# Kernel tuning notes

Hardware: AMD Instinct MI355X
Metric: run time of the kernel (lower is better)

Reference implementation:

```python
import jax, jax.numpy as jnp
import numpy as np

INV_L_MIN, INV_L_MAX = 0.5, 2.0

def _gelu(x):
    return jax.nn.gelu(x, approximate=False)

def _scaled_sigmoid(x, lo, hi):
    return lo + (hi - lo) * jax.nn.sigmoid(x)

def _fourier_bases(nodes, modes):
    # nodes: [b, n, d]; modes: [k, d, w] -> temp: [b, n, k, w]
    temp = 2.0 * jnp.pi * jnp.einsum('bxd,kdw->bxkw', nodes, modes)
    return jnp.cos(temp), jnp.sin(temp), jnp.ones_like(temp[:, :, :1, :])

def _spectral_conv(x, wc, ws, w0, bc, bs, b0, wbc, wbs, wb0):
    # x: [b, c_in, n]; forward non-uniform Fourier transform via weighted bases
    x_c = jnp.einsum('bix,bxkw->bikw', x, wbc)
    x_s = -jnp.einsum('bix,bxkw->bikw', x, wbs)
    x_0 = jnp.einsum('bix,bxkw->bikw', x, wb0)
    f_c = jnp.einsum('bikw,iokw->bokw', x_c, wc) - jnp.einsum('bikw,iokw->bokw', x_s, ws)
    f_s = jnp.einsum('bikw,iokw->bokw', x_s, wc) + jnp.einsum('bikw,iokw->bokw', x_c, ws)
    f_0 = jnp.einsum('bikw,iokw->bokw', x_0, w0)
    return (jnp.einsum('bokw,bxkw->box', f_0, b0)
            + 2.0 * jnp.einsum('bokw,bxkw->box', f_c, bc)
            - 2.0 * jnp.einsum('bokw,bxkw->box', f_s, bs))


def setup_inputs() -> dict:
    key = jax.random.key(0)
    ks = jax.random.split(key, 32)
    B, NU, NV = 4, 65536, 16384
    K, D, W = 32, 2, 1          # nmodes, ndims, nmeasures
    C, L = 64, 3                # channels, number of BNO layers
    FC, IU, IV, OUT = 128, 2, 3, 1
    f32 = jnp.float32
    rn = lambda k, s, sc=1.0: (sc * jax.random.normal(k, s, dtype=f32))
    ru = lambda k, s, sc=1.0: (sc * jax.random.uniform(k, s, dtype=f32))
    sp_scale = 1.0 / (C * C)
    inp = {
        'u': rn(ks[0], (B, NU, IU)),
        'v': rn(ks[1], (B, NV, IV)),
        'node_mask_u': jnp.ones((B, NU, 1), dtype=jnp.int32),
        'nodes_u': ru(ks[2], (B, NU, D)),
        'nodes_v': ru(ks[3], (B, NV, D)),
        'node_weights_u': ru(ks[4], (B, NU, W), 1.0 / NU),
        'node_weights_v': ru(ks[5], (B, NV, W), 1.0 / NV),
        'modes': ru(ks[6], (K, D, W), 8.0),
        # scaled_logit(1.0, 0.5, 2.0) = log((1-0.5)/(2-1)) = log(0.5)
        'inv_L_scale_latent': jnp.full((D, W), -0.69314718, dtype=f32),
        'fc0_u_w': rn(ks[7], (C, IU), 0.5), 'fc0_u_b': rn(ks[8], (C,), 0.1),
        'fc0_v_w': rn(ks[9], (C, IV), 0.5), 'fc0_v_b': rn(ks[10], (C,), 0.1),
        'sp_ext_wc': ru(ks[11], (L, C, C, K, W), sp_scale),
        'sp_ext_ws': ru(ks[12], (L, C, C, K, W), sp_scale),
        'sp_ext_w0': ru(ks[13], (L, C, C, 1, W), sp_scale),
        'sp_u_wc': ru(ks[14], (L, C, C, K, W), sp_scale),
        'sp_u_ws': ru(ks[15], (L, C, C, K, W), sp_scale),
        'sp_u_w0': ru(ks[16], (L, C, C, 1, W), sp_scale),
        'sp_v_wc': ru(ks[17], (L, C, C, K, W), sp_scale),
        'sp_v_ws': ru(ks[18], (L, C, C, K, W), sp_scale),
        'sp_v_w0': ru(ks[19], (L, C, C, 1, W), sp_scale),
        'ws_u_w': rn(ks[20], (L, C, C), 0.05), 'ws_u_b': rn(ks[21], (L, C), 0.02),
        'ws_v_w': rn(ks[22], (L, C, C), 0.05), 'ws_v_b': rn(ks[23], (L, C), 0.02),
        'fc1_w': rn(ks[24], (FC, C), 0.05), 'fc1_b': rn(ks[25], (FC,), 0.02),
        'fc2_w': rn(ks[26], (OUT, FC), 0.05), 'fc2_b': rn(ks[27], (OUT,), 0.02),
    }
    return inp


def reference(u, v, node_mask_u, nodes_u, nodes_v, node_weights_u, node_weights_v,
              modes, inv_L_scale_latent, fc0_u_w, fc0_u_b, fc0_v_w, fc0_v_b,
              sp_ext_wc, sp_ext_ws, sp_ext_w0, sp_u_wc, sp_u_ws, sp_u_w0,
              sp_v_wc, sp_v_ws, sp_v_w0, ws_u_w, ws_u_b, ws_v_w, ws_v_b,
              fc1_w, fc1_b, fc2_w, fc2_b):
    # node_mask_u is unpacked but unused in the original forward
    m = modes * _scaled_sigmoid(inv_L_scale_latent, INV_L_MIN, INV_L_MAX)  # [k,d,w]
    bc_u, bs_u, b0_u = _fourier_bases(nodes_u, m)
    bc_v, bs_v, b0_v = _fourier_bases(nodes_v, m)
    wu = node_weights_u[:, :, None, :]  # [b,x,1,w]
    wv = node_weights_v[:, :, None, :]
    wbc_u, wbs_u, wb0_u = bc_u * wu, bs_u * wu, b0_u * wu
    wbc_v, wbs_v, wb0_v = bc_v * wv, bs_v * wv, b0_v * wv
    # lift to channel dim and move to [b, c, n]
    u = jnp.einsum('bxi,oi->box', u, fc0_u_w) + fc0_u_b[None, :, None]
    v = jnp.einsum('bxi,oi->box', v, fc0_v_w) + fc0_v_b[None, :, None]
    L = ws_u_w.shape[0]
    for i in range(L):
        u1 = _spectral_conv(v, sp_ext_wc[i], sp_ext_ws[i], sp_ext_w0[i],
                            bc_u, bs_u, b0_u, wbc_v, wbs_v, wb0_v)
        u2 = _spectral_conv(u, sp_u_wc[i], sp_u_ws[i], sp_u_w0[i],
                            bc_u, bs_u, b0_u, wbc_u, wbs_u, wb0_u)
        u3 = jnp.einsum('oi,bix->box', ws_u_w[i], u) + ws_u_b[i][None, :, None]
        u = u1 + u2 + u3
        if i != L - 1:  # v is only updated on non-final layers, as in the original
            u = _gelu(u)
            v1 = _spectral_conv(v, sp_v_wc[i], sp_v_ws[i], sp_v_w0[i],
                                bc_v, bs_v, b0_v, wbc_v, wbs_v, wb0_v)
            v2 = jnp.einsum('oi,bix->box', ws_v_w[i], v) + ws_v_b[i][None, :, None]
            v = _gelu(v1 + v2)
    u = jnp.transpose(u, (0, 2, 1))  # [b, n, c]
    u = _gelu(u @ fc1_w.T + fc1_b)
    return u @ fc2_w.T + fc2_b
```

## Files before the change

### kernel.cpp

```cpp
#include <hip/hip_runtime.h>
#include <math.h>

#define PI2 6.283185307179586f

typedef __attribute__((ext_vector_type(8))) short bf16x8;
typedef __attribute__((ext_vector_type(4))) float f32x4;

__device__ __forceinline__ float gelu_f(float x) {
    return 0.5f * x * (1.0f + erff(x * 0.7071067811865476f));
}
__device__ __forceinline__ unsigned short f2bf(float f) {
    unsigned int u = __float_as_uint(f);
    u += 0x7FFFu + ((u >> 16) & 1u);
    return (unsigned short)(u >> 16);
}
__device__ __forceinline__ float bf2f(unsigned short h) {
    return __uint_as_float(((unsigned int)h) << 16);
}
__device__ __forceinline__ unsigned int pk(unsigned short a, unsigned short b) {
    return (unsigned int)a | ((unsigned int)b << 16);
}
__device__ __forceinline__ void wsplit(float w, unsigned short* dst) {
    unsigned short h = f2bf(w);
    dst[0] = h;
    dst[128] = f2bf(w - bf2f(h));
}

template<int NIN>
__global__ __launch_bounds__(256) void k_prep(const float* __restrict__ nodes, const float* __restrict__ modes,
                                              const float* __restrict__ latent, const float* __restrict__ nw,
                                              const float* __restrict__ inp, const float* __restrict__ fcw,
                                              const float* __restrict__ fcb,
                                              unsigned short* __restrict__ FT, unsigned short* __restrict__ wbb,
                                              unsigned short* __restrict__ chbf, int N) {
    int b = blockIdx.y;
    int x = blockIdx.x * 256 + threadIdx.x;
    float s0 = 0.5f + 1.5f / (1.0f + expf(-latent[0]));
    float s1 = 0.5f + 1.5f / (1.0f + expf(-latent[1]));
    float n0 = nodes[((size_t)b * N + x) * 2 + 0];
    float n1 = nodes[((size_t)b * N + x) * 2 + 1];
    float wx = nw[(size_t)b * N + x];
    unsigned short* wb = wbb + (size_t)b * 65 * N + x;
    unsigned int row[64];
    #pragma unroll
    for (int k = 0; k < 32; ++k) {
        float m0 = modes[k * 2 + 0] * s0;
        float m1 = modes[k * 2 + 1] * s1;
        float t = PI2 * (n0 * m0 + n1 * m1);
        float s, c;
        sincosf(t, &s, &c);
        unsigned short hc = f2bf(c), hs = f2bf(s);
        if (k & 1) { row[k >> 1] |= ((unsigned int)hc << 16); row[16 + (k >> 1)] |= ((unsigned int)hs << 16); }
        else       { row[k >> 1] = hc;                         row[16 + (k >> 1)] = hs; }
        wb[(size_t)k * N] = f2bf(c * wx);
        wb[(size_t)(32 + k) * N] = f2bf(s * wx);
    }
    wb[(size_t)64 * N] = f2bf(wx);
    float xi[NIN];
    #pragma unroll
    for (int i = 0; i < NIN; ++i) xi[i] = inp[((size_t)b * N + x) * NIN + i];
    unsigned short* cb = chbf + (size_t)b * 64 * N + x;
    #pragma unroll
    for (int c = 0; c < 64; ++c) {
        float a = fcb[c];
        #pragma unroll
        for (int i = 0; i < NIN; ++i) a += fcw[c * NIN + i] * xi[i];
        unsigned short h = f2bf(a);
        cb[(size_t)c * N] = h;
        if (c & 1) row[32 + (c >> 1)] |= ((unsigned int)h << 16);
        else row[32 + (c >> 1)] = h;
    }
    unsigned int* fr = (unsigned int*)(FT + ((size_t)b * N + x) * 128);
    #pragma unroll
    for (int i = 0; i < 64; ++i) fr[i] = row[i];
}

__global__ __launch_bounds__(256) void k_analysis2(const unsigned short* __restrict__ chbf_u,
                                                   const unsigned short* __restrict__ wbb_u,
                                                   const unsigned short* __restrict__ chbf_v,
                                                   const unsigned short* __restrict__ wbb_v,
                                                   float* __restrict__ part_u, float* __restrict__ part_v,
                                                   int NU_, int NV_, int chu, int chv) {
    int b = blockIdx.y, bx = blockIdx.x, tid = threadIdx.x;
    const unsigned short *chb, *wb;
    float* pb;
    int N, xlen, chunk;
    if (bx < chu) {
        chunk = bx; N = NU_; xlen = NU_ / chu;
        chb = chbf_u + (size_t)b * 64 * N;
        wb = wbb_u + (size_t)b * 65 * N;
        pb = part_u + (size_t)(b * chu + chunk) * 64 * 66;
    } else {
        chunk = bx - chu; N = NV_; xlen = NV_ / chv;
        chb = chbf_v + (size_t)b * 64 * N;
        wb = wbb_v + (size_t)b * 65 * N;
        pb = part_v + (size_t)(b * chv + chunk) * 64 * 66;
    }
    int lane = tid & 63, wv = tid >> 6;
    int lm = lane & 15, lg = lane >> 4;
    int ro = wv * 16;
    int x0 = chunk * xlen;
    f32x4 acc[5] = {};
    for (int x = x0; x < x0 + xlen; x += 32) {
        bf16x8 a = *(const bf16x8*)(chb + (size_t)(ro + lm) * N + x + lg * 8);
        #pragma unroll
        for (int ct = 0; ct < 4; ++ct) {
            bf16x8 bf = *(const bf16x8*)(wb + (size_t)(ct * 16 + lm) * N + x + lg * 8);
            acc[ct] = __builtin_amdgcn_mfma_f32_16x16x32_bf16(a, bf, acc[ct], 0, 0, 0);
        }
        bf16x8 wf = *(const bf16x8*)(wb + (size_t)64 * N + x + lg * 8);
        acc[4] = __builtin_amdgcn_mfma_f32_16x16x32_bf16(a, wf, acc[4], 0, 0, 0);
    }
    #pragma unroll
    for (int ct = 0; ct < 4; ++ct)
        #pragma unroll
        for (int j = 0; j < 4; ++j)
            pb[(ro + lg * 4 + j) * 66 + ct * 16 + lm] = acc[ct][j];
    if (lm == 0) {
        #pragma unroll
        for (int j = 0; j < 4; ++j) pb[(ro + lg * 4 + j) * 66 + 64] = acc[4][j];
    }
}

__global__ __launch_bounds__(256) void k_reduce2(const float* __restrict__ part_u, const float* __restrict__ part_v,
                                                 float* __restrict__ momu, float* __restrict__ momv,
                                                 int chu, int chv, int B_) {
    int by = blockIdx.y;
    const float* p;
    float* m;
    int nch, b;
    if (by < B_) { b = by; p = part_u; m = momu; nch = chu; }
    else { b = by - B_; p = part_v; m = momv; nch = chv; }
    int eg = threadIdx.x >> 3;
    int sp = threadIdx.x & 7;
    int e = blockIdx.x * 32 + eg;
    __shared__ float red[32][8];
    float s = 0.f;
    int row = 0, col = 0;
    if (e < 64 * 65) {
        row = e / 65; col = e % 65;
        const float* pp = p + ((size_t)(b * nch) * 64 + row) * 66 + col;
        for (int c = sp; c < nch; c += 8)
            s += pp[(size_t)c * 64 * 66];
    }
    red[eg][sp] = s;
    __syncthreads();
    if (sp == 0 && e < 64 * 65) {
        float t = 0.f;
        #pragma unroll
        for (int i = 0; i < 8; ++i) t += red[eg][i];
        m[((size_t)b * 64 + row) * 66 + col] = t;
    }
}

__global__ __launch_bounds__(256) void k_tw(const float* __restrict__ e_c, const float* __restrict__ e_s,
                                            const float* __restrict__ u_c, const float* __restrict__ u_s,
                                            const float* __restrict__ v_c, const float* __restrict__ v_s,
                                            float* __restrict__ oT) {
    int li = blockIdx.x;
    int a = blockIdx.y;
    const float* in;
    switch (a) {
        case 0: in = e_c; break;
        case 1: in = e_s; break;
        case 2: in = u_c; break;
        case 3: in = u_s; break;
        case 4: in = v_c; break;
        default: in = v_s; break;
    }
    float* outp = oT + (size_t)a * 393216;
    int l = li >> 6, i = li & 63;
    __shared__ float t[32][65];
    int tid = threadIdx.x;
    const float* ib = in + (size_t)l * 131072 + (size_t)i * 2048;
    #pragma unroll
    for (int r = 0; r < 8; ++r) {
        int e = r * 256 + tid;
        t[e & 31][e >> 5] = ib[e];
    }
    __syncthreads();
    float* ob = outp + (size_t)l * 131072 + (size_t)i * 64;
    #pragma unroll
    for (int r = 0; r < 8; ++r) {
        int e = r * 256 + tid;
        ob[(size_t)(e >> 6) * 4096 + (e & 63)] = t[e >> 6][e & 63];
    }
}

__global__ void k_buildW(const float* __restrict__ momu, const float* __restrict__ momv,
                         const float* __restrict__ ecT, const float* __restrict__ esT, const float* __restrict__ ew0,
                         const float* __restrict__ ucT, const float* __restrict__ usT, const float* __restrict__ uw0,
                         const float* __restrict__ vcT, const float* __restrict__ vsT, const float* __restrict__ vw0,
                         const float* __restrict__ wsuw, const float* __restrict__ wsub,
                         const float* __restrict__ wsvw, const float* __restrict__ wsvb,
                         unsigned short* __restrict__ WuBf, unsigned short* __restrict__ WvBf,
                         float* __restrict__ biasU, float* __restrict__ biasV, int do_v) {
    int b = blockIdx.y, j = blockIdx.x, o = threadIdx.x;
    const float* mu = momu + (size_t)b * 64 * 66;
    const float* mv = momv + (size_t)b * 64 * 66;
    unsigned short* Wub = WuBf + ((size_t)b * 64 + o) * 256;
    unsigned short* Wvb = WvBf + ((size_t)b * 64 + o) * 256;
    if (j < 32) {
        int k = j;
        const float* ec = ecT + (size_t)k * 4096;
        const float* es = esT + (size_t)k * 4096;
        const float* uc = ucT + (size_t)k * 4096;
        const float* us = usT + (size_t)k * 4096;
        const float* vc = vcT + (size_t)k * 4096;
        const float* vs = vsT + (size_t)k * 4096;
        float fcu = 0, fsu = 0, fcv = 0, fsv = 0;
        for (int i = 0; i < 64; ++i) {
            float Scv = mv[i * 66 + k], Ssv = mv[i * 66 + 32 + k];
            float Scu = mu[i * 66 + k], Ssu = mu[i * 66 + 32 + k];
            int wi = i * 64 + o;
            float e_c = ec[wi], e_s = es[wi];
            float u_c = uc[wi], u_s = us[wi];
            fcu += Scv * e_c + Ssv * e_s + Scu * u_c + Ssu * u_s;
            fsu += Scv * e_s - Ssv * e_c + Scu * u_s - Ssu * u_c;
            if (do_v) {
                float v_c = vc[wi], v_s = vs[wi];
                fcv += Scv * v_c + Ssv * v_s;
                fsv += Scv * v_s - Ssv * v_c;
            }
        }
        wsplit(2.f * fcu, Wub + k);
        wsplit(-2.f * fsu, Wub + 32 + k);
        if (do_v) {
            wsplit(2.f * fcv, Wvb + k);
            wsplit(-2.f * fsv, Wvb + 32 + k);
        }
    } else {
        for (int c = 0; c < 64; ++c) wsplit(wsuw[o * 64 + c], Wub + 64 + c);
        float f0u = 0;
        for (int i = 0; i < 64; ++i)
            f0u += mv[i * 66 + 64] * ew0[i * 64 + o] + mu[i * 66 + 64] * uw0[i * 64 + o];
        biasU[b * 64 + o] = f0u + wsub[o];
        if (do_v) {
            for (int c = 0; c < 64; ++c) wsplit(wsvw[o * 64 + c], Wvb + 64 + c);
            float f0v = 0;
            for (int i = 0; i < 64; ++i) f0v += mv[i * 66 + 64] * vw0[i * 64 + o];
            biasV[b * 64 + o] = f0v + wsvb[o];
        }
    }
}

__global__ void k_buildW_slow(const float* __restrict__ momu, const float* __restrict__ momv,
                              const float* __restrict__ ewc, const float* __restrict__ ews, const float* __restrict__ ew0,
                              const float* __restrict__ uwc, const float* __restrict__ uws, const float* __restrict__ uw0,
                              const float* __restrict__ vwc, const float* __restrict__ vws, const float* __restrict__ vw0,
                              const float* __restrict__ wsuw, const float* __restrict__ wsub,
                              const float* __restrict__ wsvw, const float* __restrict__ wsvb,
                              unsigned short* __restrict__ WuBf, unsigned short* __restrict__ WvBf,
                              float* __restrict__ biasU, float* __restrict__ biasV, int do_v) {
    int b = blockIdx.y, j = blockIdx.x, o = threadIdx.x;
    const float* mu = momu + (size_t)b * 64 * 66;
    const float* mv = momv + (size_t)b * 64 * 66;
    unsigned short* Wub = WuBf + ((size_t)b * 64 + o) * 256;
    unsigned short* Wvb = WvBf + ((size_t)b * 64 + o) * 256;
    if (j < 32) {
        int k = j;
        float fcu = 0, fsu = 0, fcv = 0, fsv = 0;
        for (int i = 0; i < 64; ++i) {
            float Scv = mv[i * 66 + k], Ssv = mv[i * 66 + 32 + k];
            float Scu = mu[i * 66 + k], Ssu = mu[i * 66 + 32 + k];
            int wi = (i * 64 + o) * 32 + k;
            float ec = ewc[wi], es = ews[wi];
            float uc = uwc[wi], us = uws[wi];
            fcu += Scv * ec + Ssv * es + Scu * uc + Ssu * us;
            fsu += Scv * es - Ssv * ec + Scu * us - Ssu * uc;
            if (do_v) {
                float vc = vwc[wi], vs = vws[wi];
                fcv += Scv * vc + Ssv * vs;
                fsv += Scv * vs - Ssv * vc;
            }
        }
        wsplit(2.f * fcu, Wub + k);
        wsplit(-2.f * fsu, Wub + 32 + k);
        if (do_v) {
            wsplit(2.f * fcv, Wvb + k);
            wsplit(-2.f * fsv, Wvb + 32 + k);
        }
    } else {
        for (int c = 0; c < 64; ++c) wsplit(wsuw[o * 64 + c], Wub + 64 + c);
        float f0u = 0;
        for (int i = 0; i < 64; ++i)
            f0u += mv[i * 66 + 64] * ew0[i * 64 + o] + mu[i * 66 + 64] * uw0[i * 64 + o];
        biasU[b * 64 + o] = f0u + wsub[o];
        if (do_v) {
            for (int c = 0; c < 64; ++c) wsplit(wsvw[o * 64 + c], Wvb + 64 + c);
            float f0v = 0;
            for (int i = 0; i < 64; ++i) f0v += mv[i * 66 + 64] * vw0[i * 64 + o];
            biasV[b * 64 + o] = f0v + wsvb[o];
        }
    }
}

__global__ __launch_bounds__(256) void k_synth3(const unsigned short* __restrict__ WuBf,
                                                const unsigned short* __restrict__ WvBf,
                                                const float* __restrict__ biasU, const float* __restrict__ biasV,
                                                unsigned short* FTu, unsigned short* FTv,
                                                const unsigned short* __restrict__ wbb_u,
                                                const unsigned short* __restrict__ wbb_v,
                                                float* __restrict__ part_u, float* __restrict__ part_v,
                                                int NU_, int NV_, int nbu, int act_u, int wft_v, int do_mom) {
    int bx = blockIdx.x, b = blockIdx.y, tid = threadIdx.x;
    const unsigned short* Wb;
    const float* bi;
    unsigned short* FT;
    const unsigned short* wb;
    float* pb;
    int N, act, wft, blk;
    if (bx < nbu) {
        blk = bx; Wb = WuBf; bi = biasU; FT = FTu; N = NU_;
        wb = wbb_u + (size_t)b * 65 * NU_;
        pb = part_u + (size_t)(b * (NU_ / 128) + blk) * 64 * 66;
        act = act_u; wft = 1;
    } else {
        blk = bx - nbu; Wb = WvBf; bi = biasV; FT = FTv; N = NV_;
        wb = wbb_v + (size_t)b * 65 * NV_;
        pb = part_v + (size_t)(b * (NV_ / 128) + blk) * 64 * 66;
        act = 1; wft = wft_v;
    }
    int lane = tid & 63, wv = tid >> 6;
    int lm = lane & 15, lg = lane >> 4;
    int ro = wv * 16;
    const unsigned short* Wrow = Wb + ((size_t)b * 64 + ro + lm) * 256;
    bf16x8 ahi[4], alo[4];
    #pragma unroll
    for (int kt = 0; kt < 4; ++kt) {
        ahi[kt] = *(const bf16x8*)(Wrow + kt * 32 + lg * 8);
        alo[kt] = *(const bf16x8*)(Wrow + 128 + kt * 32 + lg * 8);
    }
    float bias[4];
    #pragma unroll
    for (int j = 0; j < 4; ++j) bias[j] = bi[b * 64 + ro + lg * 4 + j];
    unsigned short* ftb = FT + (size_t)b * N * 128;
    __shared__ unsigned short st2[64][136];
    int r0 = ro + lg * 4;
    int x0 = blk * 128;
    f32x4 acc[8] = {};
    #pragma unroll
    for (int xt = 0; xt < 8; ++xt) {
        int x = x0 + xt * 16 + lm;
        const unsigned short* fp = ftb + (size_t)x * 128 + lg * 8;
        #pragma unroll
        for (int kt = 0; kt < 4; ++kt) {
            bf16x8 bf = *(const bf16x8*)(fp + kt * 32);
            acc[xt] = __builtin_amdgcn_mfma_f32_16x16x32_bf16(ahi[kt], bf, acc[xt], 0, 0, 0);
            acc[xt] = __builtin_amdgcn_mfma_f32_16x16x32_bf16(alo[kt], bf, acc[xt], 0, 0, 0);
        }
    }
    __syncthreads();
    #pragma unroll
    for (int xt = 0; xt < 8; ++xt) {
        int xl = xt * 16 + lm;
        float v[4];
        #pragma unroll
        for (int j = 0; j < 4; ++j) {
            v[j] = acc[xt][j] + bias[j];
            if (act) v[j] = gelu_f(v[j]);
        }
        unsigned short h[4];
        #pragma unroll
        for (int j = 0; j < 4; ++j) h[j] = f2bf(v[j]);
        if (do_mom) {
            st2[r0 + 0][xl] = h[0];
            st2[r0 + 1][xl] = h[1];
            st2[r0 + 2][xl] = h[2];
            st2[r0 + 3][xl] = h[3];
        }
        if (wft) {
            unsigned int* dst = (unsigned int*)(ftb + (size_t)(x0 + xl) * 128 + 64 + r0);
            dst[0] = pk(h[0], h[1]);
            dst[1] = pk(h[2], h[3]);
        }
    }
    if (do_mom) {
        __syncthreads();
        f32x4 macc[5] = {};
        #pragma unroll
        for (int xs = 0; xs < 128; xs += 32) {
            bf16x8 a = *(const bf16x8*)&st2[ro + lm][xs + lg * 8];
            #pragma unroll
            for (int ct = 0; ct < 4; ++ct) {
                bf16x8 bw = *(const bf16x8*)(wb + (size_t)(ct * 16 + lm) * N + x0 + xs + lg * 8);
                macc[ct] = __builtin_amdgcn_mfma_f32_16x16x32_bf16(a, bw, macc[ct], 0, 0, 0);
            }
            bf16x8 wf = *(const bf16x8*)(wb + (size_t)64 * N + x0 + xs + lg * 8);
            macc[4] = __builtin_amdgcn_mfma_f32_16x16x32_bf16(a, wf, macc[4], 0, 0, 0);
        }
        #pragma unroll
        for (int ct = 0; ct < 4; ++ct)
            #pragma unroll
            for (int j = 0; j < 4; ++j)
                pb[(r0 + j) * 66 + ct * 16 + lm] = macc[ct][j];
        if (lm == 0) {
            #pragma unroll
            for (int j = 0; j < 4; ++j) pb[(r0 + j) * 66 + 64] = macc[4][j];
        }
    }
}

__global__ __launch_bounds__(256) void k_fc12(const unsigned short* __restrict__ FT, const float* __restrict__ w1,
                                              const float* __restrict__ b1, const float* __restrict__ w2,
                                              const float* __restrict__ b2, float* __restrict__ out, int N) {
    int b = blockIdx.y, blk = blockIdx.x, tid = threadIdx.x;
    int lane = tid & 63, wv = tid >> 6;
    int lm = lane & 15, lg = lane >> 4;
    int f0 = wv * 32;
    bf16x8 ahi[2][2], alo[2][2];
    #pragma unroll
    for (int ft = 0; ft < 2; ++ft)
        #pragma unroll
        for (int kt = 0; kt < 2; ++kt) {
            const float* wp = w1 + (size_t)(f0 + ft * 16 + lm) * 64 + kt * 32 + lg * 8;
            float tmp[8];
            *(float4*)&tmp[0] = *(const float4*)wp;
            *(float4*)&tmp[4] = *(const float4*)(wp + 4);
            #pragma unroll
            for (int i = 0; i < 8; ++i) {
                unsigned short h = f2bf(tmp[i]);
                ahi[ft][kt][i] = (short)h;
                alo[ft][kt][i] = (short)f2bf(tmp[i] - bf2f(h));
            }
        }
    float b1v[2][4], w2v[2][4];
    #pragma unroll
    for (int ft = 0; ft < 2; ++ft)
        #pragma unroll
        for (int j = 0; j < 4; ++j) {
            int f = f0 + ft * 16 + lg * 4 + j;
            b1v[ft][j] = b1[f];
            w2v[ft][j] = w2[f];
        }
    f32x4 acc[8][2] = {};
    const unsigned short* ftb = FT + (size_t)b * N * 128;
    int x0 = blk * 128;
    #pragma unroll
    for (int xt = 0; xt < 8; ++xt) {
        const unsigned short* fp = ftb + (size_t)(x0 + xt * 16 + lm) * 128 + 64 + lg * 8;
        bf16x8 bf0 = *(const bf16x8*)fp;
        bf16x8 bf1 = *(const bf16x8*)(fp + 32);
        #pragma unroll
        for (int ft = 0; ft < 2; ++ft) {
            acc[xt][ft] = __builtin_amdgcn_mfma_f32_16x16x32_bf16(ahi[ft][0], bf0, acc[xt][ft], 0, 0, 0);
            acc[xt][ft] = __builtin_amdgcn_mfma_f32_16x16x32_bf16(alo[ft][0], bf0, acc[xt][ft], 0, 0, 0);
            acc[xt][ft] = __builtin_amdgcn_mfma_f32_16x16x32_bf16(ahi[ft][1], bf1, acc[xt][ft], 0, 0, 0);
            acc[xt][ft] = __builtin_amdgcn_mfma_f32_16x16x32_bf16(alo[ft][1], bf1, acc[xt][ft], 0, 0, 0);
        }
    }
    __shared__ float red[4][8][16];
    #pragma unroll
    for (int xt = 0; xt < 8; ++xt) {
        float s = 0.f;
        #pragma unroll
        for (int ft = 0; ft < 2; ++ft)
            #pragma unroll
            for (int j = 0; j < 4; ++j) {
                float v = acc[xt][ft][j] + b1v[ft][j];
                s += w2v[ft][j] * gelu_f(v);
            }
        s += __shfl_xor(s, 16, 64);
        s += __shfl_xor(s, 32, 64);
        if (lg == 0) red[wv][xt][lm] = s;
    }
    __syncthreads();
    if (tid < 128) {
        int xt = tid >> 4, lmm = tid & 15;
        float s = b2[0] + red[0][xt][lmm] + red[1][xt][lmm] + red[2][xt][lmm] + red[3][xt][lmm];
        out[(size_t)b * N + x0 + tid] = s;
    }
}

extern "C" void kernel_launch(void* const* d_in, const int* in_sizes, int n_in,
                              void* d_out, int out_size, void* d_ws, size_t ws_size,
                              hipStream_t stream) {
    const float* u_in = (const float*)d_in[0];
    const float* v_in = (const float*)d_in[1];
    const float* nodes_u = (const float*)d_in[3];
    const float* nodes_v = (const float*)d_in[4];
    const float* nwu = (const float*)d_in[5];
    const float* nwv = (const float*)d_in[6];
    const float* modes = (const float*)d_in[7];
    const float* latent = (const float*)d_in[8];
    const float* fc0uw = (const float*)d_in[9];
    const float* fc0ub = (const float*)d_in[10];
    const float* fc0vw = (const float*)d_in[11];
    const float* fc0vb = (const float*)d_in[12];
    const float* ewc = (const float*)d_in[13];
    const float* ews = (const float*)d_in[14];
    const float* ew0 = (const float*)d_in[15];
    const float* uwc = (const float*)d_in[16];
    const float* uws = (const float*)d_in[17];
    const float* uw0 = (const float*)d_in[18];
    const float* vwc = (const float*)d_in[19];
    const float* vws = (const float*)d_in[20];
    const float* vw0 = (const float*)d_in[21];
    const float* wsuw = (const float*)d_in[22];
    const float* wsub = (const float*)d_in[23];
    const float* wsvw = (const float*)d_in[24];
    const float* wsvb = (const float*)d_in[25];
    const float* fc1w = (const float*)d_in[26];
    const float* fc1b = (const float*)d_in[27];
    const float* fc2w = (const float*)d_in[28];
    const float* fc2b = (const float*)d_in[29];
    float* out = (float*)d_out;

    const int B = 4, NU = 65536, NV = 16384;
    const int CH_U0 = 256, CH_V0 = 128;
    const int CH_UL = NU / 128, CH_VL = NV / 128;

    unsigned short* FT_u = (unsigned short*)d_ws;
    unsigned short* FT_v = FT_u + (size_t)B * NU * 128;
    unsigned short* wbb_u = FT_v + (size_t)B * NV * 128;
    unsigned short* wbb_v = wbb_u + (size_t)B * 65 * NU;
    unsigned short* chbf_u = wbb_v + (size_t)B * 65 * NV;
    unsigned short* chbf_v = chbf_u + (size_t)B * 64 * NU;
    float* slotA = (float*)(chbf_v + (size_t)B * 64 * NV);
    float* slotB = slotA + (size_t)B * CH_U0 * 64 * 66;
    float* momu = slotB + (size_t)B * CH_V0 * 64 * 66;
    float* momv = momu + B * 64 * 66;
    unsigned short* WuBf = (unsigned short*)(momv + B * 64 * 66);
    unsigned short* WvBf = WuBf + (size_t)B * 64 * 256;
    float* biasU = (float*)(WvBf + (size_t)B * 64 * 256);
    float* biasV = biasU + B * 64;
    float* wT = biasV + B * 64;
    size_t need_T = (size_t)((char*)(wT + 6 * 393216) - (char*)d_ws);
    int use_T = (ws_size >= need_T) ? 1 : 0;

    float* part0_u = slotA;
    float* part0_v = slotB;
    float* partL_u = (float*)chbf_u;
    float* partL_v = slotA;

    k_prep<2><<<dim3(NU / 256, B), 256, 0, stream>>>(nodes_u, modes, latent, nwu, u_in, fc0uw, fc0ub,
                                                     FT_u, wbb_u, chbf_u, NU);
    k_prep<3><<<dim3(NV / 256, B), 256, 0, stream>>>(nodes_v, modes, latent, nwv, v_in, fc0vw, fc0vb,
                                                     FT_v, wbb_v, chbf_v, NV);
    if (use_T)
        k_tw<<<dim3(192, 6), 256, 0, stream>>>(ewc, ews, uwc, uws, vwc, vws, wT);

    k_analysis2<<<dim3(CH_U0 + CH_V0, B), 256, 0, stream>>>(chbf_u, wbb_u, chbf_v, wbb_v,
                                                            part0_u, part0_v, NU, NV, CH_U0, CH_V0);

    for (int l = 0; l < 3; ++l) {
        int do_v = (l < 2) ? 1 : 0;
        const float* ru = (l == 0) ? part0_u : partL_u;
        const float* rv = (l == 0) ? part0_v : partL_v;
        int chu_l = (l == 0) ? CH_U0 : CH_UL;
        int chv_l = (l == 0) ? CH_V0 : CH_VL;
        k_reduce2<<<dim3(130, 2 * B), 256, 0, stream>>>(ru, rv, momu, momv, chu_l, chv_l, B);
        if (use_T) {
            k_buildW<<<dim3(33, B), 64, 0, stream>>>(momu, momv,
                wT + 0 * 393216 + l * 131072, wT + 1 * 393216 + l * 131072, ew0 + (size_t)l * 64 * 64,
                wT + 2 * 393216 + l * 131072, wT + 3 * 393216 + l * 131072, uw0 + (size_t)l * 64 * 64,
                wT + 4 * 393216 + l * 131072, wT + 5 * 393216 + l * 131072, vw0 + (size_t)l * 64 * 64,
                wsuw + l * 64 * 64, wsub + l * 64, wsvw + l * 64 * 64, wsvb + l * 64,
                WuBf, WvBf, biasU, biasV, do_v);
        } else {
            k_buildW_slow<<<dim3(33, B), 64, 0, stream>>>(momu, momv,
                ewc + (size_t)l * 64 * 64 * 32, ews + (size_t)l * 64 * 64 * 32, ew0 + (size_t)l * 64 * 64,
                uwc + (size_t)l * 64 * 64 * 32, uws + (size_t)l * 64 * 64 * 32, uw0 + (size_t)l * 64 * 64,
                vwc + (size_t)l * 64 * 64 * 32, vws + (size_t)l * 64 * 64 * 32, vw0 + (size_t)l * 64 * 64,
                wsuw + l * 64 * 64, wsub + l * 64, wsvw + l * 64 * 64, wsvb + l * 64,
                WuBf, WvBf, biasU, biasV, do_v);
        }
        int nbu = NU / 128;
        int nbx = nbu + (do_v ? NV / 128 : 0);
        int do_mom = (l < 2) ? 1 : 0;
        int wft_v = (l == 0) ? 1 : 0;
        k_synth3<<<dim3(nbx, B), 256, 0, stream>>>(WuBf, WvBf, biasU, biasV, FT_u, FT_v,
                                                   wbb_u, wbb_v, partL_u, partL_v,
                                                   NU, NV, nbu, do_v , wft_v, do_mom);
    }
    k_fc12<<<dim3(NU / 128, B), 256, 0, stream>>>(FT_u, fc1w, fc1b, fc2w, fc2b, out, NU);
}
```

Baseline: 504.8 us.

## Fuse initial analysis GEMM into prep kernel via shared-memory staging

The prep kernel now handles 128 nodes per block with two thread halves splitting modes and channels. It stages the lifted channels and weighted bases in LDS and runs the first analysis MFMA directly, writing per-block partial moments. This removes the separate analysis kernel and the global round trip for the bf16 channel buffer. Partials now use 128-node chunks everywhere, so the first reduce reads more partials than the old 256/128-chunk layout, and LDS use grows.

```diff
diff --git a/kernel.cpp b/kernel.cpp
--- a/kernel.cpp
+++ b/kernel.cpp
@@ -32,85 +32,80 @@
                                               const float* __restrict__ inp, const float* __restrict__ fcw,
                                               const float* __restrict__ fcb,
                                               unsigned short* __restrict__ FT, unsigned short* __restrict__ wbb,
-                                              unsigned short* __restrict__ chbf, int N) {
+                                              float* __restrict__ part, int N) {
     int b = blockIdx.y;
-    int x = blockIdx.x * 256 + threadIdx.x;
+    int tid = threadIdx.x;
+    int xl = tid & 127, half = tid >> 7;
+    int x = blockIdx.x * 128 + xl;
+    __shared__ unsigned short st_c[64][136];
+    __shared__ unsigned short st_w[65][136];
     float s0 = 0.5f + 1.5f / (1.0f + expf(-latent[0]));
     float s1 = 0.5f + 1.5f / (1.0f + expf(-latent[1]));
     float n0 = nodes[((size_t)b * N + x) * 2 + 0];
     float n1 = nodes[((size_t)b * N + x) * 2 + 1];
     float wx = nw[(size_t)b * N + x];
     unsigned short* wb = wbb + (size_t)b * 65 * N + x;
-    unsigned int row[64];
-    #pragma unroll
-    for (int k = 0; k < 32; ++k) {
+    unsigned int fcos[8], fsin[8], fch[16];
+    #pragma unroll
+    for (int kk = 0; kk < 16; ++kk) {
+        int k = half * 16 + kk;
         float m0 = modes[k * 2 + 0] * s0;
         float m1 = modes[k * 2 + 1] * s1;
         float t = PI2 * (n0 * m0 + n1 * m1);
         float s, c;
         sincosf(t, &s, &c);
         unsigned short hc = f2bf(c), hs = f2bf(s);
-        if (k & 1) { row[k >> 1] |= ((unsigned int)hc << 16); row[16 + (k >> 1)] |= ((unsigned int)hs << 16); }
-        else       { row[k >> 1] = hc;                         row[16 + (k >> 1)] = hs; }
-        wb[(size_t)k * N] = f2bf(c * wx);
-        wb[(size_t)(32 + k) * N] = f2bf(s * wx);
-    }
-    wb[(size_t)64 * N] = f2bf(wx);
+        if (kk & 1) { fcos[kk >> 1] |= ((unsigned int)hc << 16); fsin[kk >> 1] |= ((unsigned int)hs << 16); }
+        else        { fcos[kk >> 1] = hc;                         fsin[kk >> 1] = hs; }
+        unsigned short hcw = f2bf(c * wx), hsw = f2bf(s * wx);
+        st_w[k][xl] = hcw;
+        st_w[32 + k][xl] = hsw;
+        wb[(size_t)k * N] = hcw;
+        wb[(size_t)(32 + k) * N] = hsw;
+    }
+    if (half) {
+        unsigned short hw = f2bf(wx);
+        st_w[64][xl] = hw;
+        wb[(size_t)64 * N] = hw;
+    }
     float xi[NIN];
     #pragma unroll
     for (int i = 0; i < NIN; ++i) xi[i] = inp[((size_t)b * N + x) * NIN + i];
-    unsigned short* cb = chbf + (size_t)b * 64 * N + x;
-    #pragma unroll
-    for (int c = 0; c < 64; ++c) {
+    #pragma unroll
+    for (int cc = 0; cc < 32; ++cc) {
+        int c = half * 32 + cc;
         float a = fcb[c];
         #pragma unroll
         for (int i = 0; i < NIN; ++i) a += fcw[c * NIN + i] * xi[i];
         unsigned short h = f2bf(a);
-        cb[(size_t)c * N] = h;
-        if (c & 1) row[32 + (c >> 1)] |= ((unsigned int)h << 16);
-        else row[32 + (c >> 1)] = h;
+        st_c[c][xl] = h;
+        if (cc & 1) fch[cc >> 1] |= ((unsigned int)h << 16);
+        else fch[cc >> 1] = h;
     }
     unsigned int* fr = (unsigned int*)(FT + ((size_t)b * N + x) * 128);
     #pragma unroll
-    for (int i = 0; i < 64; ++i) fr[i] = row[i];
-}
-
-__global__ __launch_bounds__(256) void k_analysis2(const unsigned short* __restrict__ chbf_u,
-                                                   const unsigned short* __restrict__ wbb_u,
-                                                   const unsigned short* __restrict__ chbf_v,
-                                                   const unsigned short* __restrict__ wbb_v,
-                                                   float* __restrict__ part_u, float* __restrict__ part_v,
-                                                   int NU_, int NV_, int chu, int chv) {
-    int b = blockIdx.y, bx = blockIdx.x, tid = threadIdx.x;
-    const unsigned short *chb, *wb;
-    float* pb;
-    int N, xlen, chunk;
-    if (bx < chu) {
-        chunk = bx; N = NU_; xlen = NU_ / chu;
-        chb = chbf_u + (size_t)b * 64 * N;
-        wb = wbb_u + (size_t)b * 65 * N;
-        pb = part_u + (size_t)(b * chu + chunk) * 64 * 66;
-    } else {
-        chunk = bx - chu; N = NV_; xlen = NV_ / chv;
-        chb = chbf_v + (size_t)b * 64 * N;
-        wb = wbb_v + (size_t)b * 65 * N;
-        pb = part_v + (size_t)(b * chv + chunk) * 64 * 66;
-    }
+    for (int i = 0; i < 8; ++i) fr[half * 8 + i] = fcos[i];
+    #pragma unroll
+    for (int i = 0; i < 8; ++i) fr[16 + half * 8 + i] = fsin[i];
+    #pragma unroll
+    for (int i = 0; i < 16; ++i) fr[32 + half * 16 + i] = fch[i];
+    __syncthreads();
     int lane = tid & 63, wv = tid >> 6;
     int lm = lane & 15, lg = lane >> 4;
     int ro = wv * 16;
-    int x0 = chunk * xlen;
     f32x4 acc[5] = {};
-    for (int x = x0; x < x0 + xlen; x += 32) {
-        bf16x8 a = *(const bf16x8*)(chb + (size_t)(ro + lm) * N + x + lg * 8);
+    #pragma unroll
+    for (int xs = 0; xs < 128; xs += 32) {
+        bf16x8 a = *(const bf16x8*)&st_c[ro + lm][xs + lg * 8];
         #pragma unroll
         for (int ct = 0; ct < 4; ++ct) {
-            bf16x8 bf = *(const bf16x8*)(wb + (size_t)(ct * 16 + lm) * N + x + lg * 8);
-            acc[ct] = __builtin_amdgcn_mfma_f32_16x16x32_bf16(a, bf, acc[ct], 0, 0, 0);
-        }
-        bf16x8 wf = *(const bf16x8*)(wb + (size_t)64 * N + x + lg * 8);
+            bf16x8 bw = *(const bf16x8*)&st_w[ct * 16 + lm][xs + lg * 8];
+            acc[ct] = __builtin_amdgcn_mfma_f32_16x16x32_bf16(a, bw, acc[ct], 0, 0, 0);
+        }
+        bf16x8 wf = *(const bf16x8*)&st_w[64][xs + lg * 8];
         acc[4] = __builtin_amdgcn_mfma_f32_16x16x32_bf16(a, wf, acc[4], 0, 0, 0);
     }
+    float* pb = part + (size_t)(b * (N / 128) + blockIdx.x) * 64 * 66;
     #pragma unroll
     for (int ct = 0; ct < 4; ++ct)
         #pragma unroll
@@ -507,18 +502,15 @@
     float* out = (float*)d_out;
 
     const int B = 4, NU = 65536, NV = 16384;
-    const int CH_U0 = 256, CH_V0 = 128;
-    const int CH_UL = NU / 128, CH_VL = NV / 128;
+    const int CH_U = NU / 128, CH_V = NV / 128;
 
     unsigned short* FT_u = (unsigned short*)d_ws;
     unsigned short* FT_v = FT_u + (size_t)B * NU * 128;
     unsigned short* wbb_u = FT_v + (size_t)B * NV * 128;
     unsigned short* wbb_v = wbb_u + (size_t)B * 65 * NU;
-    unsigned short* chbf_u = wbb_v + (size_t)B * 65 * NV;
-    unsigned short* chbf_v = chbf_u + (size_t)B * 64 * NU;
-    float* slotA = (float*)(chbf_v + (size_t)B * 64 * NV);
-    float* slotB = slotA + (size_t)B * CH_U0 * 64 * 66;
-    float* momu = slotB + (size_t)B * CH_V0 * 64 * 66;
+    float* part_u = (float*)(wbb_v + (size_t)B * 65 * NV);
+    float* part_v = part_u + (size_t)B * CH_U * 64 * 66;
+    float* momu = part_v + (size_t)B * CH_V * 64 * 66;
     float* momv = momu + B * 64 * 66;
     unsigned short* WuBf = (unsigned short*)(momv + B * 64 * 66);
     unsigned short* WvBf = WuBf + (size_t)B * 64 * 256;
@@ -528,28 +520,16 @@
     size_t need_T = (size_t)((char*)(wT + 6 * 393216) - (char*)d_ws);
     int use_T = (ws_size >= need_T) ? 1 : 0;
 
-    float* part0_u = slotA;
-    float* part0_v = slotB;
-    float* partL_u = (float*)chbf_u;
-    float* partL_v = slotA;
-
-    k_prep<2><<<dim3(NU / 256, B), 256, 0, stream>>>(nodes_u, modes, latent, nwu, u_in, fc0uw, fc0ub,
-                                                     FT_u, wbb_u, chbf_u, NU);
-    k_prep<3><<<dim3(NV / 256, B), 256, 0, stream>>>(nodes_v, modes, latent, nwv, v_in, fc0vw, fc0vb,
-                                                     FT_v, wbb_v, chbf_v, NV);
+    k_prep<2><<<dim3(NU / 128, B), 256, 0, stream>>>(nodes_u, modes, latent, nwu, u_in, fc0uw, fc0ub,
+                                                     FT_u, wbb_u, part_u, NU);
+    k_prep<3><<<dim3(NV / 128, B), 256, 0, stream>>>(nodes_v, modes, latent, nwv, v_in, fc0vw, fc0vb,
+                                                     FT_v, wbb_v, part_v, NV);
     if (use_T)
         k_tw<<<dim3(192, 6), 256, 0, stream>>>(ewc, ews, uwc, uws, vwc, vws, wT);
 
-    k_analysis2<<<dim3(CH_U0 + CH_V0, B), 256, 0, stream>>>(chbf_u, wbb_u, chbf_v, wbb_v,
-                                                            part0_u, part0_v, NU, NV, CH_U0, CH_V0);
-
     for (int l = 0; l < 3; ++l) {
         int do_v = (l < 2) ? 1 : 0;
-        const float* ru = (l == 0) ? part0_u : partL_u;
-        const float* rv = (l == 0) ? part0_v : partL_v;
-        int chu_l = (l == 0) ? CH_U0 : CH_UL;
-        int chv_l = (l == 0) ? CH_V0 : CH_VL;
-        k_reduce2<<<dim3(130, 2 * B), 256, 0, stream>>>(ru, rv, momu, momv, chu_l, chv_l, B);
+        k_reduce2<<<dim3(130, 2 * B), 256, 0, stream>>>(part_u, part_v, momu, momv, CH_U, CH_V, B);
         if (use_T) {
             k_buildW<<<dim3(33, B), 64, 0, stream>>>(momu, momv,
                 wT + 0 * 393216 + l * 131072, wT + 1 * 393216 + l * 131072, ew0 + (size_t)l * 64 * 64,
@@ -570,7 +550,7 @@
         int do_mom = (l < 2) ? 1 : 0;
         int wft_v = (l == 0) ? 1 : 0;
         k_synth3<<<dim3(nbx, B), 256, 0, stream>>>(WuBf, WvBf, biasU, biasV, FT_u, FT_v,
-                                                   wbb_u, wbb_v, partL_u, partL_v,
+                                                   wbb_u, wbb_v, part_u, part_v,
                                                    NU, NV, nbu, do_v , wft_v, do_mom);
     }
     k_fc12<<<dim3(NU / 128, B), 256, 0, stream>>>(FT_u, fc1w, fc1b, fc2w, fc2b, out, NU);
```

Result: faster. 482.6 us (-4.4%).
